# Kernel tuning notes

Measured on AMD Instinct MI355X. Metric: run time of the kernel, lower is better.

Reference implementation:

```python
import jax, jax.numpy as jnp
import numpy as np

T, B, E, H = 1024, 4, 1024, 16
Dh = E // H
NEG_INF = float('-inf')


def setup_inputs() -> dict:
    key = jax.random.key(0)
    k1, k2, k3, k4 = jax.random.split(key, 4)
    return {
        'fwd_x': jax.random.normal(k1, (T, B, E), jnp.float32),
        'bwd_x': jax.random.normal(k2, (T, B, E), jnp.float32),
        'in_proj_weight': jax.random.normal(k3, (3 * E, E), jnp.float32) * 0.02,
        'in_proj_bias': jnp.zeros((3 * E,), jnp.float32),
        'out_w': jax.random.normal(k4, (E, E), jnp.float32) * 0.02,
        'out_b': jnp.zeros((E,), jnp.float32),
    }


def reference(fwd_x, bwd_x, in_proj_weight, in_proj_bias, out_w, out_b):
    t, b, e = fwd_x.shape
    s = 2 * t
    dtype = fwd_x.dtype
    zeros = jnp.zeros((1, b, e), dtype)
    # padded_fwd_x[0:t] -> [0, fwd_x[:-1]]; padded_bwd_x[1:t+1] -> [bwd_x[1:], 0]
    q_in = jnp.concatenate([zeros, fwd_x[:-1]], 0) + jnp.concatenate([bwd_x[1:], zeros], 0)
    kv = jnp.concatenate([fwd_x, bwd_x], 0)  # [s, b, e]

    wq, wk, wv = in_proj_weight[:e], in_proj_weight[e:2 * e], in_proj_weight[2 * e:]
    bq, bk, bv = in_proj_bias[:e], in_proj_bias[e:2 * e], in_proj_bias[2 * e:]
    q = (q_in @ wq.T + bq).reshape(t, b, H, Dh)
    k = (kv @ wk.T + bk).reshape(s, b, H, Dh)
    v = (kv @ wv.T + bv).reshape(s, b, H, Dh)

    # NOTE: original module never applies self.scaling in forward -- keep unscaled.
    attn_weights = jnp.einsum('tbhd,sbhd->bhts', q, k)  # [b, H, t, s]

    # mask_curr_state=True: allowed keys are j < i (fwd half) or j > i + t (bwd half)
    i = jnp.arange(t)[:, None]
    j = jnp.arange(s)[None, :]
    allowed = (j >= i + t + 1) | (j <= i - 1)
    mask_bias = jnp.where(allowed, 0.0, NEG_INF).astype(dtype)
    attn_weights = attn_weights + mask_bias[None, None]

    probs = jax.nn.softmax(attn_weights.astype(jnp.float32), axis=-1).astype(dtype)

    attn = jnp.einsum('bhts,sbhd->tbhd', probs, v).reshape(t, b, e)
    attn = attn @ out_w.T + out_b
    avg_weights = probs.mean(axis=1)  # [b, t, s]
    return attn, avg_weights
```

## Files before the change

### kernel.cpp

```cpp
#include <hip/hip_runtime.h>

typedef unsigned short u16;
typedef __attribute__((ext_vector_type(8))) short short8;
typedef __attribute__((ext_vector_type(4))) float f32x4;

#define SM_SHIFT 24.0f

__device__ __forceinline__ u16 f2b(float f) {
  unsigned u = __float_as_uint(f);
  unsigned r = (u + 0x7FFFu + ((u >> 16) & 1u)) >> 16;
  return (u16)r;
}

__device__ __forceinline__ void gload16(const u16* g, u16* l) {
  __builtin_amdgcn_global_load_lds((const __attribute__((address_space(1))) void*)g,
                                   (__attribute__((address_space(3))) void*)l, 16, 0, 0);
}

__device__ __forceinline__ void cast4(const float* __restrict__ src,
                                      u16* __restrict__ dst, int gid) {
  float4 v = *(const float4*)(src + (gid << 2));
  ushort4 o; o.x = f2b(v.x); o.y = f2b(v.y); o.z = f2b(v.z); o.w = f2b(v.w);
  *(ushort4*)(dst + (gid << 2)) = o;
}

__global__ __launch_bounds__(256) void prep_all(const float* __restrict__ fwd,
                                                const float* __restrict__ bwd,
                                                const float* __restrict__ w_in,
                                                const float* __restrict__ w_out,
                                                u16* __restrict__ qin,
                                                u16* __restrict__ kvf,
                                                u16* __restrict__ kvb,
                                                u16* __restrict__ wbf,
                                                u16* __restrict__ wobf) {
  const int blk = blockIdx.x, tid = threadIdx.x;
  if (blk < 4096) {
    int gid = blk * 256 + tid;
    int n = gid >> 8;
    int e4 = (gid & 255) << 2;
    int t = n >> 2, b = n & 3;
    float4 acc = make_float4(0.f, 0.f, 0.f, 0.f);
    if (t > 0) {
      float4 v = *(const float4*)(fwd + (((t - 1) * 4 + b) << 10) + e4);
      acc.x += v.x; acc.y += v.y; acc.z += v.z; acc.w += v.w;
    }
    if (t < 1023) {
      float4 v = *(const float4*)(bwd + (((t + 1) * 4 + b) << 10) + e4);
      acc.x += v.x; acc.y += v.y; acc.z += v.z; acc.w += v.w;
    }
    ushort4 o; o.x = f2b(acc.x); o.y = f2b(acc.y); o.z = f2b(acc.z); o.w = f2b(acc.w);
    *(ushort4*)(qin + (n << 10) + e4) = o;
  } else if (blk < 8192) {
    cast4(fwd, kvf, (blk - 4096) * 256 + tid);
  } else if (blk < 12288) {
    cast4(bwd, kvb, (blk - 8192) * 256 + tid);
  } else if (blk < 15360) {
    cast4(w_in, wbf, (blk - 12288) * 256 + tid);
  } else {
    cast4(w_out, wobf, (blk - 15360) * 256 + tid);
  }
}

__global__ __launch_bounds__(512, 2) void gemm_kv256(const u16* __restrict__ A,
                                                     const u16* __restrict__ W,
                                                     const float* __restrict__ bias,
                                                     u16* __restrict__ outK,
                                                     u16* __restrict__ outV) {
  __shared__ u16 SH[65536];
  const int x = blockIdx.x & 7, local = blockIdx.x >> 3;
  const int mt = x * 4 + (local & 3);
  const int nt = local >> 2;
  const int m0 = mt << 8, n0 = nt << 8;
  const int tid = threadIdx.x;
  const int lane = tid & 63, wid = tid >> 6;
  const int wm = (wid >> 2) << 7;
  const int wn = (wid & 3) << 6;
  const int lr = lane & 15, lg = lane >> 4;
  const int scol = (lane & 7) << 3;
  const int swc = ((lane & 7) ^ (lane >> 3)) << 3;
  f32x4 acc[8][4] = {};
  auto At = [&](int buf) { return SH + buf * 16384; };
  auto Wt = [&](int buf) { return SH + 32768 + buf * 16384; };
  auto stage = [&](int buf, int k0) {
    u16* a = At(buf); u16* w = Wt(buf);
#pragma unroll
    for (int it = 0; it < 4; it++) {
      int row = (it * 8 + wid) * 8 + (lane >> 3);
      gload16(&A[(size_t)(m0 + row) * 1024 + k0 + swc], &a[row * 64 + scol]);
      gload16(&W[(size_t)(n0 + row) * 1024 + k0 + swc], &w[row * 64 + scol]);
    }
  };
  auto compute = [&](int buf) {
    const u16* a = At(buf); const u16* w = Wt(buf);
#pragma unroll
    for (int kk = 0; kk < 64; kk += 32) {
      int co = (((kk >> 3) + lg) ^ (lr & 7)) << 3;
      short8 af[8], bf[4];
#pragma unroll
      for (int i = 0; i < 8; i++)
        af[i] = *(const short8*)&a[(wm + i * 16 + lr) * 64 + co];
#pragma unroll
      for (int j = 0; j < 4; j++)
        bf[j] = *(const short8*)&w[(wn + j * 16 + lr) * 64 + co];
#pragma unroll
      for (int i = 0; i < 8; i++)
#pragma unroll
        for (int j = 0; j < 4; j++)
          acc[i][j] = __builtin_amdgcn_mfma_f32_16x16x32_bf16(af[i], bf[j], acc[i][j], 0, 0, 0);
    }
  };
  stage(0, 0);
  __syncthreads();
  for (int step = 0; step < 16; ++step) {
    const int cur = step & 1;
    if (step < 15) stage(cur ^ 1, (step + 1) << 6);
    compute(cur);
    __syncthreads();
  }
  u16* C = SH;
#pragma unroll
  for (int i = 0; i < 8; i++) {
#pragma unroll
    for (int j = 0; j < 4; j++) {
      int n = wn + j * 16 + lr;
      float bv = bias[n0 + n];
      int np = n ^ (lg << 4);
#pragma unroll
      for (int r = 0; r < 4; r++) {
        int m = wm + i * 16 + lg * 4 + r;
        C[m * 256 + np] = f2b(acc[i][j][r] + bv);
      }
    }
  }
  __syncthreads();
  const bool isK = (n0 < 1024);
  u16* ob = isK ? outK : outV;
  const int hbase = isK ? (n0 >> 6) : ((n0 - 1024) >> 6);
  const int ts0 = m0 >> 2;
  const int ts = tid >> 3, c8d = tid & 7;
#pragma unroll
  for (int k = 0; k < 16; ++k) {
    int tb = k >> 2, hh = k & 3;
    int m = ts * 4 + tb;
    int c8 = (hh * 8 + c8d) ^ ((ts & 3) << 1);
    uint4 val = *(const uint4*)&C[m * 256 + c8 * 8];
    size_t off = ((size_t)(tb * 16 + hbase + hh) * 2048 + ts0 + ts) * 64 + c8d * 8;
    *(uint4*)&ob[off] = val;
  }
}

template <int MODE, int MTX>
__global__ __launch_bounds__(256) void gemm_bt(const u16* __restrict__ A,
                                               const u16* __restrict__ W,
                                               const float* __restrict__ bias,
                                               void* __restrict__ outp) {
  __shared__ u16 At[2][128 * 64];
  __shared__ u16 Wt[2][128 * 64];
  const int x = blockIdx.x & 7, local = blockIdx.x >> 3;
  const int mt = x * MTX + (local % MTX);
  const int nt = local / MTX;
  const int m0 = mt << 7, n0 = nt << 7;
  const int tid = threadIdx.x;
  const int lane = tid & 63, wid = tid >> 6;
  const int wm = (wid >> 1) << 6, wn = (wid & 1) << 6;
  const int lr = lane & 15, lg = lane >> 4;
  const int srow = lane >> 3, scol = (lane & 7) << 3;
  const int swc = ((lane & 7) ^ srow) << 3;
  f32x4 acc[4][4] = {};
  auto stage = [&](int buf, int k0) {
#pragma unroll
    for (int it = 0; it < 4; it++) {
      int row = (it * 4 + wid) * 8 + srow;
      gload16(&A[(m0 + row) * 1024 + k0 + swc], &At[buf][row * 64 + scol]);
      gload16(&W[(n0 + row) * 1024 + k0 + swc], &Wt[buf][row * 64 + scol]);
    }
  };
  auto compute = [&](int buf) {
#pragma unroll
    for (int kk = 0; kk < 64; kk += 32) {
      short8 af[4], bf[4];
#pragma unroll
      for (int i = 0; i < 4; i++) {
        int co = (((kk >> 3) + lg) ^ (lr & 7)) << 3;
        af[i] = *(const short8*)&At[buf][(wm + i * 16 + lr) * 64 + co];
        bf[i] = *(const short8*)&Wt[buf][(wn + i * 16 + lr) * 64 + co];
      }
#pragma unroll
      for (int i = 0; i < 4; i++)
#pragma unroll
        for (int j = 0; j < 4; j++)
          acc[i][j] = __builtin_amdgcn_mfma_f32_16x16x32_bf16(af[i], bf[j], acc[i][j], 0, 0, 0);
    }
  };
  stage(0, 0);
  __syncthreads();
  for (int step = 0; step < 16; ++step) {
    const int cur = step & 1;
    if (step < 15) stage(cur ^ 1, (step + 1) << 6);
    compute(cur);
    __syncthreads();
  }
#pragma unroll
  for (int i = 0; i < 4; i++) {
#pragma unroll
    for (int j = 0; j < 4; j++) {
      int n = n0 + wn + j * 16 + lr;
      float bv = bias[n];
#pragma unroll
      for (int r = 0; r < 4; r++) {
        int m = m0 + wm + i * 16 + lg * 4 + r;
        float v = acc[i][j][r] + bv;
        if (MODE == 3) {
          ((float*)outp)[m * 1024 + n] = v;
        } else {
          int tb = m & 3, ts = m >> 2, hh = n >> 6, d = n & 63;
          ((u16*)outp)[((tb * 16 + hh) * 1024 + ts) * 64 + d] = f2b(v);
        }
      }
    }
  }
}

__global__ __launch_bounds__(256) void transpose_v(const u16* __restrict__ v,
                                                   u16* __restrict__ vt) {
  __shared__ u16 L[64 * 66];
  const int blk = blockIdx.x;
  const int bh = blk >> 5, s0 = (blk & 31) << 6;
  const int tid = threadIdx.x;
  const u16* src = v + ((size_t)bh * 2048 + s0) * 64;
  u16* dst = vt + (size_t)bh * 64 * 2048 + s0;
#pragma unroll
  for (int it = 0; it < 2; ++it) {
    int idx = it * 256 + tid;
    int sl = idx >> 3, dc = (idx & 7) << 3;
    short8 v8 = *(const short8*)&src[sl * 64 + dc];
#pragma unroll
    for (int e = 0; e < 8; ++e)
      L[(dc + e) * 66 + sl] = (u16)v8[e];
  }
  __syncthreads();
#pragma unroll
  for (int it = 0; it < 2; ++it) {
    int idx = it * 256 + tid;
    int dr = idx >> 3, sc = (idx & 7) << 3;
    *(short8*)&dst[(size_t)dr * 2048 + sc] = *(const short8*)&L[dr * 66 + sc];
  }
}

__global__ __launch_bounds__(256) void attn_fwd(const u16* __restrict__ qb,
                                                const u16* __restrict__ kb,
                                                const u16* __restrict__ vtb,
                                                u16* __restrict__ attn_bf,
                                                float* __restrict__ st_il) {
  __shared__ u16 Kt[64 * 64];
  __shared__ u16 Vt[64 * 64];
  __shared__ u16 Pt[4][16 * 72];
  const int g = blockIdx.x;
  const int L = ((g & 7) << 7) | (g >> 3);
  const int t0 = (L & 15) << 6;
  const int h = (L >> 4) & 15;
  const int b = L >> 8;
  const int tid = threadIdx.x, lane = tid & 63, w = tid >> 6;
  const int lr = lane & 15, lg = lane >> 4;
  const int bh = b * 16 + h;
  const int sw0 = ((lg ^ (lr & 7)) << 3);
  const int sw1 = sw0 ^ 32;
  const u16* qrow = qb + ((bh << 10) + t0 + (w << 4) + lr) * 64;
  short8 qf0 = *(const short8*)&qrow[lg * 8];
  short8 qf1 = *(const short8*)&qrow[32 + lg * 8];
  const u16* kbase = kb + (size_t)(bh << 11) * 64;
  const u16* vbase = vtb + (size_t)(bh << 6) * 2048;
  f32x4 acc[4] = {};
  f32x4 accl = {};
  const int n1 = (t0 >> 6) + 1;
  const int grow = lane >> 3, gcol = (lane & 7) << 3;
  short8 ones;
#pragma unroll
  for (int j = 0; j < 8; ++j) ones[j] = (short)0x3F80;
  for (int ti = 0; ti < 17; ++ti) {
    const int s0 = (ti < n1) ? (ti << 6) : (t0 + 1024 + ((ti - n1) << 6));
    __syncthreads();
#pragma unroll
    for (int it = 0; it < 2; ++it) {
      int row = (it * 4 + w) * 8 + grow;
      int swc = (((lane & 7) ^ (row & 7)) << 3);
      gload16(&kbase[(size_t)(s0 + row) * 64 + swc], &Kt[row * 64 + gcol]);
      gload16(&vbase[(size_t)row * 2048 + s0 + swc], &Vt[row * 64 + gcol]);
    }
    __syncthreads();
    float pv[4][4];
#pragma unroll
    for (int c = 0; c < 4; c++) {
      f32x4 sc = {};
      short8 kf0 = *(const short8*)&Kt[(c * 16 + lr) * 64 + sw0];
      short8 kf1 = *(const short8*)&Kt[(c * 16 + lr) * 64 + sw1];
      sc = __builtin_amdgcn_mfma_f32_16x16x32_bf16(qf0, kf0, sc, 0, 0, 0);
      sc = __builtin_amdgcn_mfma_f32_16x16x32_bf16(qf1, kf1, sc, 0, 0, 0);
      int j = s0 + c * 16 + lr;
#pragma unroll
      for (int r = 0; r < 4; r++) {
        int i = t0 + (w << 4) + lg * 4 + r;
        float e = __expf(sc[r] - SM_SHIFT);
        pv[c][r] = ((j < i) || (j > i + 1024)) ? e : 0.f;
      }
    }
#pragma unroll
    for (int c = 0; c < 4; c++)
#pragma unroll
      for (int r = 0; r < 4; r++)
        Pt[w][(lg * 4 + r) * 72 + c * 16 + lr] = f2b(pv[c][r]);
    short8 pf0 = *(const short8*)&Pt[w][lr * 72 + lg * 8];
    short8 pf1 = *(const short8*)&Pt[w][lr * 72 + 32 + lg * 8];
    accl = __builtin_amdgcn_mfma_f32_16x16x32_bf16(pf0, ones, accl, 0, 0, 0);
    accl = __builtin_amdgcn_mfma_f32_16x16x32_bf16(pf1, ones, accl, 0, 0, 0);
#pragma unroll
    for (int dd = 0; dd < 4; dd++) {
      short8 vf0 = *(const short8*)&Vt[(dd * 16 + lr) * 64 + sw0];
      short8 vf1 = *(const short8*)&Vt[(dd * 16 + lr) * 64 + sw1];
      acc[dd] = __builtin_amdgcn_mfma_f32_16x16x32_bf16(pf0, vf0, acc[dd], 0, 0, 0);
      acc[dd] = __builtin_amdgcn_mfma_f32_16x16x32_bf16(pf1, vf1, acc[dd], 0, 0, 0);
    }
  }
  float inv[4];
#pragma unroll
  for (int r = 0; r < 4; r++) inv[r] = 1.f / accl[r];
  const int trow = t0 + (w << 4) + lg * 4;
#pragma unroll
  for (int dd = 0; dd < 4; dd++)
#pragma unroll
    for (int r = 0; r < 4; r++)
      attn_bf[((trow + r) * 4 + b) * 1024 + h * 64 + dd * 16 + lr] = f2b(acc[dd][r] * inv[r]);
#pragma unroll
  for (int r = 0; r < 4; r++)
    if (lr == r)
      st_il[(bh << 10) + trow + r] = inv[r];
}

__global__ __launch_bounds__(256) void attn_avg(const u16* __restrict__ qb,
                                                const u16* __restrict__ kb,
                                                const float* __restrict__ st_il,
                                                float* __restrict__ avg) {
  __shared__ u16 Kt[2][128 * 64];
  __shared__ float Si[16][64];
  const int g = blockIdx.x;
  const int L = ((g & 7) << 7) | (g >> 3);
  const int s0 = (L & 15) << 7;
  const int t0 = ((L >> 4) & 15) << 6;
  const int b = L >> 8;
  const int tid = threadIdx.x, lane = tid & 63, w = tid >> 6;
  const int lr = lane & 15, lg = lane >> 4;
  const int trow = t0 + (w << 4) + lg * 4;
  float* obase = avg + (size_t)b * (1024 * 2048);
  if ((s0 > t0 + 62) && (s0 + 127 < t0 + 1025)) {
#pragma unroll
    for (int c = 0; c < 8; c++)
#pragma unroll
      for (int r = 0; r < 4; r++)
        obase[(trow + r) * 2048 + s0 + c * 16 + lr] = 0.f;
    return;
  }
  for (int i = tid; i < 1024; i += 256) {
    int hh = i >> 6, tt = i & 63;
    Si[hh][tt] = st_il[(((b << 4) + hh) << 10) + t0 + tt];
  }
  const int sw0 = ((lg ^ (lr & 7)) << 3);
  const int sw1 = sw0 ^ 32;
  const int grow = lane >> 3, gcol = (lane & 7) << 3;
  const int srr = (w << 4) + lg * 4;
  auto stage = [&](int buf, int hh) {
    const u16* kb_h = kb + ((size_t)(((b << 4) + hh) << 11) + s0) * 64;
#pragma unroll
    for (int it = 0; it < 4; ++it) {
      int row = (it * 4 + w) * 8 + grow;
      int swc = (((lane & 7) ^ (row & 7)) << 3);
      gload16(&kb_h[(size_t)row * 64 + swc], &Kt[buf][row * 64 + gcol]);
    }
  };
  stage(0, 0);
  __syncthreads();
  float accv[8][4] = {};
  for (int h = 0; h < 16; h++) {
    const int cur = h & 1;
    if (h < 15) stage(cur ^ 1, h + 1);
    const int bh = (b << 4) + h;
    const u16* qrow = qb + ((bh << 10) + t0 + (w << 4) + lr) * 64;
    short8 qf0 = *(const short8*)&qrow[lg * 8];
    short8 qf1 = *(const short8*)&qrow[32 + lg * 8];
    float ih[4];
#pragma unroll
    for (int r = 0; r < 4; r++) ih[r] = Si[h][srr + r];
#pragma unroll
    for (int c = 0; c < 8; c++) {
      int c0 = s0 + (c << 4);
      if (c0 >= t0 + 63 && c0 <= t0 + 1009) continue;
      f32x4 sc = {};
      short8 kf0 = *(const short8*)&Kt[cur][(c * 16 + lr) * 64 + sw0];
      short8 kf1 = *(const short8*)&Kt[cur][(c * 16 + lr) * 64 + sw1];
      sc = __builtin_amdgcn_mfma_f32_16x16x32_bf16(qf0, kf0, sc, 0, 0, 0);
      sc = __builtin_amdgcn_mfma_f32_16x16x32_bf16(qf1, kf1, sc, 0, 0, 0);
      int j = c0 + lr;
#pragma unroll
      for (int r = 0; r < 4; r++) {
        int i = t0 + (w << 4) + lg * 4 + r;
        if ((j < i) || (j > i + 1024))
          accv[c][r] += __expf(sc[r] - SM_SHIFT) * ih[r];
      }
    }
    __syncthreads();
  }
#pragma unroll
  for (int c = 0; c < 8; c++)
#pragma unroll
    for (int r = 0; r < 4; r++)
      obase[(trow + r) * 2048 + s0 + c * 16 + lr] = accv[c][r] * 0.0625f;
}

extern "C" void kernel_launch(void* const* d_in, const int* in_sizes, int n_in,
                              void* d_out, int out_size, void* d_ws, size_t ws_size,
                              hipStream_t stream) {
  const float* fwd   = (const float*)d_in[0];
  const float* bwd   = (const float*)d_in[1];
  const float* w_in  = (const float*)d_in[2];
  const float* b_in  = (const float*)d_in[3];
  const float* w_out = (const float*)d_in[4];
  const float* b_out = (const float*)d_in[5];

  char* ws = (char*)d_ws;
  u16*  q_in_bf = (u16*)(ws);
  u16*  kv_bf   = (u16*)(ws + 8388608);
  u16*  vt_bf   = (u16*)(ws + 8388608);
  u16*  w_bf    = (u16*)(ws + 25165824);
  u16*  wo_bf   = (u16*)(ws + 31457280);
  u16*  q_bf    = (u16*)(ws + 33554432);
  u16*  k_bf    = (u16*)(ws + 41943040);
  u16*  v_tmp   = (u16*)(ws + 58720256);
  u16*  attn_bf = (u16*)(ws + 75497472);
  float* st_il  = (float*)(ws + 83886080);

  float* out_attn = (float*)d_out;
  float* out_avg  = (float*)d_out + 4194304;

  prep_all<<<16384, 256, 0, stream>>>(fwd, bwd, w_in, w_out, q_in_bf, kv_bf,
                                      kv_bf + 4194304, w_bf, wo_bf);

  gemm_bt<0, 4><<<256, 256, 0, stream>>>(q_in_bf, w_bf, b_in, (void*)q_bf);
  gemm_kv256<<<256, 512, 0, stream>>>(kv_bf, w_bf + 1048576, b_in + 1024,
                                      k_bf, v_tmp);
  transpose_v<<<2048, 256, 0, stream>>>(v_tmp, vt_bf);

  attn_fwd<<<1024, 256, 0, stream>>>(q_bf, k_bf, vt_bf, attn_bf, st_il);

  gemm_bt<3, 4><<<256, 256, 0, stream>>>(attn_bf, wo_bf, b_out,
                                         (void*)out_attn);

  attn_avg<<<1024, 256, 0, stream>>>(q_bf, k_bf, st_il, out_avg);
}
```

Before: 190.6 us.

## Shrink attn_avg tiles to 64 columns and zero masked region in prep kernel

```diff
diff --git a/kernel.cpp b/kernel.cpp
--- a/kernel.cpp
+++ b/kernel.cpp
@@ -32,7 +32,8 @@
                                                 u16* __restrict__ kvf,
                                                 u16* __restrict__ kvb,
                                                 u16* __restrict__ wbf,
-                                                u16* __restrict__ wobf) {
+                                                u16* __restrict__ wobf,
+                                                float* __restrict__ out_avg) {
   const int blk = blockIdx.x, tid = threadIdx.x;
   if (blk < 4096) {
     int gid = blk * 256 + tid;
@@ -56,8 +57,21 @@
     cast4(bwd, kvb, (blk - 8192) * 256 + tid);
   } else if (blk < 15360) {
     cast4(w_in, wbf, (blk - 12288) * 256 + tid);
+  } else if (blk < 16384) {
+    cast4(w_out, wobf, (blk - 15360) * 256 + tid);
   } else {
-    cast4(w_out, wobf, (blk - 15360) * 256 + tid);
+    int z = blk - 16384;
+    int mi = z % 15, bt2 = z / 15;
+    int tb2 = bt2 & 15, b2 = bt2 >> 4;
+    int s0z = (tb2 + 1 + mi) << 6, t0z = tb2 << 6;
+    float* ob = out_avg + (size_t)b2 * 2097152 + (size_t)t0z * 2048 + s0z;
+    float4 zz = make_float4(0.f, 0.f, 0.f, 0.f);
+#pragma unroll
+    for (int it = 0; it < 4; ++it) {
+      int idx = it * 256 + tid;
+      int rr = idx >> 4, c4 = (idx & 15) << 2;
+      *(float4*)&ob[rr * 2048 + c4] = zz;
+    }
   }
 }
 
@@ -340,25 +354,19 @@
                                                 const u16* __restrict__ kb,
                                                 const float* __restrict__ st_il,
                                                 float* __restrict__ avg) {
-  __shared__ u16 Kt[2][128 * 64];
+  __shared__ u16 Kt[2][64 * 64];
   __shared__ float Si[16][64];
   const int g = blockIdx.x;
-  const int L = ((g & 7) << 7) | (g >> 3);
-  const int s0 = (L & 15) << 7;
-  const int t0 = ((L >> 4) & 15) << 6;
-  const int b = L >> 8;
+  const int L = (g & 7) * 136 + (g >> 3);
+  const int l = L % 17;
+  const int bt = L / 17;
+  const int tb = bt & 15, b = bt >> 4;
+  const int sb = (l <= tb) ? l : l + 15;
+  const int s0 = sb << 6, t0 = tb << 6;
   const int tid = threadIdx.x, lane = tid & 63, w = tid >> 6;
   const int lr = lane & 15, lg = lane >> 4;
   const int trow = t0 + (w << 4) + lg * 4;
-  float* obase = avg + (size_t)b * (1024 * 2048);
-  if ((s0 > t0 + 62) && (s0 + 127 < t0 + 1025)) {
-#pragma unroll
-    for (int c = 0; c < 8; c++)
-#pragma unroll
-      for (int r = 0; r < 4; r++)
-        obase[(trow + r) * 2048 + s0 + c * 16 + lr] = 0.f;
-    return;
-  }
+  float* obase = avg + (size_t)b * 2097152;
   for (int i = tid; i < 1024; i += 256) {
     int hh = i >> 6, tt = i & 63;
     Si[hh][tt] = st_il[(((b << 4) + hh) << 10) + t0 + tt];
@@ -370,15 +378,15 @@
   auto stage = [&](int buf, int hh) {
     const u16* kb_h = kb + ((size_t)(((b << 4) + hh) << 11) + s0) * 64;
 #pragma unroll
-    for (int it = 0; it < 4; ++it) {
-      int row = (it * 4 + w) * 8 + grow;
-      int swc = (((lane & 7) ^ (row & 7)) << 3);
+    for (int it = 0; it < 2; ++it) {
+      int row = it * 32 + w * 8 + grow;
+      int swc = (((lane & 7) ^ grow) << 3);
       gload16(&kb_h[(size_t)row * 64 + swc], &Kt[buf][row * 64 + gcol]);
     }
   };
   stage(0, 0);
   __syncthreads();
-  float accv[8][4] = {};
+  float accv[4][4] = {};
   for (int h = 0; h < 16; h++) {
     const int cur = h & 1;
     if (h < 15) stage(cur ^ 1, h + 1);
@@ -390,15 +398,13 @@
 #pragma unroll
     for (int r = 0; r < 4; r++) ih[r] = Si[h][srr + r];
 #pragma unroll
-    for (int c = 0; c < 8; c++) {
-      int c0 = s0 + (c << 4);
-      if (c0 >= t0 + 63 && c0 <= t0 + 1009) continue;
+    for (int c = 0; c < 4; c++) {
       f32x4 sc = {};
       short8 kf0 = *(const short8*)&Kt[cur][(c * 16 + lr) * 64 + sw0];
       short8 kf1 = *(const short8*)&Kt[cur][(c * 16 + lr) * 64 + sw1];
       sc = __builtin_amdgcn_mfma_f32_16x16x32_bf16(qf0, kf0, sc, 0, 0, 0);
       sc = __builtin_amdgcn_mfma_f32_16x16x32_bf16(qf1, kf1, sc, 0, 0, 0);
-      int j = c0 + lr;
+      int j = s0 + c * 16 + lr;
 #pragma unroll
       for (int r = 0; r < 4; r++) {
         int i = t0 + (w << 4) + lg * 4 + r;
@@ -409,7 +415,7 @@
     __syncthreads();
   }
 #pragma unroll
-  for (int c = 0; c < 8; c++)
+  for (int c = 0; c < 4; c++)
 #pragma unroll
     for (int r = 0; r < 4; r++)
       obase[(trow + r) * 2048 + s0 + c * 16 + lr] = accv[c][r] * 0.0625f;
@@ -440,8 +446,8 @@
   float* out_attn = (float*)d_out;
   float* out_avg  = (float*)d_out + 4194304;
 
-  prep_all<<<16384, 256, 0, stream>>>(fwd, bwd, w_in, w_out, q_in_bf, kv_bf,
-                                      kv_bf + 4194304, w_bf, wo_bf);
+  prep_all<<<17344, 256, 0, stream>>>(fwd, bwd, w_in, w_out, q_in_bf, kv_bf,
+                                      kv_bf + 4194304, w_bf, wo_bf, out_avg);
 
   gemm_bt<0, 4><<<256, 256, 0, stream>>>(q_in_bf, w_bf, b_in, (void*)q_bf);
   gemm_kv256<<<256, 512, 0, stream>>>(kv_bf, w_bf + 1048576, b_in + 1024,
@@ -453,5 +459,5 @@
   gemm_bt<3, 4><<<256, 256, 0, stream>>>(attn_bf, wo_bf, b_out,
                                          (void*)out_attn);
 
-  attn_avg<<<1024, 256, 0, stream>>>(q_bf, k_bf, st_il, out_avg);
-}
+  attn_avg<<<1088, 256, 0, stream>>>(q_bf, k_bf, st_il, out_avg);
+}
```

New measurement: 182.8 us. 1.04x faster.
